# Kernel optimization log

Hardware: AMD Instinct MI355X
Metric: run time of the kernel (lower is better)

The kernel has to match this reference:

```python
import jax, jax.numpy as jnp
import numpy as np

GRID_SIZE = 5
SPLINE_ORDER = 3
GRID_MIN = -1.0
GRID_MAX = 1.0
H = (GRID_MAX - GRID_MIN) / GRID_SIZE          # grid interval
G0 = GRID_MIN - SPLINE_ORDER * H               # first (extended) knot = grid[:,0]


def _basis_matrix():
    # Uniform B-spline power-basis matrix, same recurrence as the torch code.
    M = np.array([[1.0]], dtype=np.float64)
    scalar = 1.0
    for k in range(2, SPLINE_ORDER + 2):
        t1 = np.pad(M, ((0, 1), (0, 0)))
        t3 = np.pad(M, ((1, 0), (0, 0)))
        t2 = np.zeros((k - 1, k))
        t4 = np.zeros((k - 1, k))
        for i in range(k - 1):
            t2[i, i] = i + 1
            t2[i, i + 1] = k - (i + 2)
            t4[i, i] = -1.0
            t4[i, i + 1] = 1.0
        M = t1 @ t2 + t3 @ t4
        scalar *= 1.0 / (k - 1)
    return (M * scalar).astype(np.float32)

BASIS = jnp.asarray(_basis_matrix())  # (spline_order+1, spline_order+1)


def setup_inputs():
    key = jax.random.key(0)
    k1, k2, k3 = jax.random.split(key, 3)
    N, FIN, FOUT = 2048, 128, 128
    x = jax.random.normal(k1, (N, FIN), dtype=jnp.float32)
    base_weight = jax.random.normal(k2, (FOUT, FIN), dtype=jnp.float32) * 0.1
    spline_weight = jax.random.normal(k3, (FIN, FOUT, GRID_SIZE + SPLINE_ORDER), dtype=jnp.float32) * 0.1
    return {"x": x, "base_weight": base_weight, "spline_weight": spline_weight}


def _forward(x, base_weight, spline_weight):
    N, fin = x.shape
    fout = base_weight.shape[0]
    k = SPLINE_ORDER
    # base branch: SiLU activation then linear
    base_out = jax.nn.silu(x) @ base_weight.T                       # (N, fout)
    # input normalization: Hardtanh around grid center (shift=0, scale=1 for [-1,1])
    shift = (GRID_MIN + GRID_MAX) / 2.0
    scale = (GRID_MAX - GRID_MIN) / 2.0
    xn = jnp.clip((x - shift) / scale, -1.0, 1.0) * scale + shift
    # bucketize: bin index + fractional position (replaces floor/compare + torch.nonzero)
    t = (xn - G0) / H
    fl = jnp.floor(t)
    u1 = t - fl                                                     # (x - interval_floor) / interval
    idx = jnp.clip(fl.astype(jnp.int32), k, k + GRID_SIZE - 1)      # clamped knot-interval index
    cfloor = idx - k                                                # (N, fin) first control point index
    # power bases [1, u, u^2, ..., u^k] -> b-spline basis via basis matrix
    pows = u1[..., None] ** jnp.arange(k + 1, dtype=x.dtype)        # (N, fin, k+1)
    bspl = pows @ BASIS.astype(x.dtype)                             # (N, fin, k+1)
    # faithful to torch: spline_weight.view(out, in, -1) memory reinterpretation
    cp = jnp.reshape(spline_weight, (fout, fin, GRID_SIZE + k))
    gidx = cfloor[..., None] + jnp.arange(k + 1)                    # (N, fin, k+1) control point indices
    i_idx = jnp.arange(fin)[None, :, None]
    gathered = cp[:, i_idx, gidx]                                   # (fout, N, fin, k+1)
    gathered = jnp.transpose(gathered, (1, 0, 2, 3))                # (N, fout, fin, k+1)
    # faithful to torch: .view(N, in, k+1, out) memory reinterpretation
    cpr = jnp.reshape(gathered, (N, fin, k + 1, fout))
    # per-feature spline matmul then sum over in_features (KAN aggregation)
    spline_out = jnp.einsum('nij,nijo->no', bspl, cpr)              # (N, fout)
    return base_out + spline_out


def reference(x, base_weight, spline_weight):
    return _forward(x, base_weight, spline_weight)
```

## Files before the change

kernel.cpp:

```cpp
#include <hip/hip_runtime.h>
#include <hip/hip_bf16.h>
#include <math.h>

typedef __attribute__((ext_vector_type(8))) short short8;
typedef __attribute__((ext_vector_type(4))) float floatx4;

static __device__ __forceinline__ unsigned short bfbits(float f) {
    __hip_bfloat16 h = __float2bfloat16(f);
    unsigned short u;
    __builtin_memcpy(&u, &h, 2);
    return u;
}
static __device__ __forceinline__ unsigned pack2(float lo, float hi) {
    return (unsigned)bfbits(lo) | ((unsigned)bfbits(hi) << 16);
}

#define SP_STR  136
#define SBN_STR 76
#define SBB_STR 136
#define ST_STR  68
#define SC_STR  132

__global__ __launch_bounds__(256) void kan_fused(
    const float* __restrict__ x,
    const float* __restrict__ bw,
    const float* __restrict__ sw,
    float* __restrict__ out)
{
    __shared__ short sP[5 * 16 * SP_STR];
    __shared__ short sBn[2][128 * SBN_STR];
    __shared__ short sBb[32 * SBB_STR];
    __shared__ float sT[2][16 * ST_STR];
    __shared__ unsigned char sC[16 * SC_STR];

    const int tid = threadIdx.x;
    const int nb  = blockIdx.x >> 2;
    const int s   = blockIdx.x & 3;
    const int n0  = nb * 16;

    const int ar = tid >> 4;
    const int sg = tid & 15;

    const int r  = tid >> 4;
    const int i0 = (tid & 15) * 8;
    float v[8];
    *(float4*)(v)     = *(const float4*)(x + (n0 + r) * 128 + i0);
    *(float4*)(v + 4) = *(const float4*)(x + (n0 + r) * 128 + i0 + 4);

    float4 pre[8];
#pragma unroll
    for (int rr = 0; rr < 8; ++rr)
        pre[rr] = *(const float4*)(sw + (ar + 16 * rr) * 1024 + s * 64 + sg * 4);

    {
        float A5[5][8];
        unsigned char cc8[8];
#pragma unroll
        for (int i = 0; i < 8; ++i) {
            float xv = v[i];
            float si = xv / (1.0f + expf(-xv));
            float xn = fminf(fmaxf(xv, -1.0f), 1.0f);
            float t  = (xn + 2.2f) / 0.4f;
            float u  = t - floorf(t);
            int idx  = (int)floorf(t);
            idx = min(max(idx, 3), 7);
            cc8[i] = (unsigned char)(idx - 3);
            float u2 = u * u, u3 = u2 * u, om = 1.0f - u;
            A5[0][i] = om * om * om * (1.0f / 6.0f);
            A5[1][i] = 0.5f * u3 - u2 + (2.0f / 3.0f);
            A5[2][i] = -0.5f * u3 + 0.5f * u2 + 0.5f * u + (1.0f / 6.0f);
            A5[3][i] = u3 * (1.0f / 6.0f);
            A5[4][i] = si;
        }
#pragma unroll
        for (int g = 0; g < 5; ++g) {
            unsigned p0 = pack2(A5[g][0], A5[g][1]);
            unsigned p1 = pack2(A5[g][2], A5[g][3]);
            unsigned p2 = pack2(A5[g][4], A5[g][5]);
            unsigned p3 = pack2(A5[g][6], A5[g][7]);
            *(uint4*)(&sP[(g * 16 + r) * SP_STR + i0]) = make_uint4(p0, p1, p2, p3);
        }
        *(unsigned*)(&sC[r * SC_STR + i0])     = cc8[0] | (cc8[1]<<8) | (cc8[2]<<16) | (cc8[3]<<24);
        *(unsigned*)(&sC[r * SC_STR + i0 + 4]) = cc8[4] | (cc8[5]<<8) | (cc8[6]<<16) | (cc8[7]<<24);
    }

    const int w = tid >> 6, l = tid & 63;
    const int m = l & 15, q = l >> 4;
    const int gn  = tid >> 4;
    const int go2 = tid & 15;

    uint2 pk[8];
#pragma unroll
    for (int rr = 0; rr < 8; ++rr)
        pk[rr] = make_uint2(pack2(pre[rr].x, pre[rr].y), pack2(pre[rr].z, pre[rr].w));

    float racc0 = 0.f, racc1 = 0.f;
    float4 bpre[4];

#pragma unroll
    for (int t = 0; t < 4; ++t) {
        const int p = t & 1;
#pragma unroll
        for (int rr = 0; rr < 8; ++rr)
            *(uint2*)(&sBn[p][(ar + 16 * rr) * SBN_STR + sg * 4]) = pk[rr];
        __syncthreads();

        if (t < 3) {
#pragma unroll
            for (int rr = 0; rr < 8; ++rr)
                pre[rr] = *(const float4*)(sw + (ar + 16 * rr) * 1024 + (s + 4 * (t + 1)) * 64 + sg * 4);
        } else {
#pragma unroll
            for (int i = 0; i < 4; ++i) {
                int e = i * 256 + tid;
                bpre[i] = *(const float4*)(bw + (32 * s + (e >> 5)) * 128 + (e & 31) * 4);
            }
        }

        if (t > 0) {
            int oh  = 8 * s + (go2 >> 1);
            int c   = sC[gn * SC_STR + 32 * (t - 1) + oh];
            int rel = 8 * (go2 >> 1) + c + 2 * (go2 & 1);
            racc0 += sT[1 - p][gn * ST_STR + rel];
            racc1 += sT[1 - p][gn * ST_STR + rel + 1];
        }

        floatx4 acc = {0.f, 0.f, 0.f, 0.f};
#pragma unroll
        for (int kk = 0; kk < 4; ++kk) {
            short8 af = *(const short8*)(&sP[(t * 16 + m) * SP_STR + q * 8 + kk * 32]);
            short8 bf;
#pragma unroll
            for (int j2 = 0; j2 < 8; ++j2)
                bf[j2] = sBn[p][(kk * 32 + q * 8 + j2) * SBN_STR + 16 * w + m];
            acc = __builtin_amdgcn_mfma_f32_16x16x32_bf16(af, bf, acc, 0, 0, 0);
        }
#pragma unroll
        for (int rr = 0; rr < 4; ++rr)
            sT[p][(q * 4 + rr) * ST_STR + 16 * w + m] = acc[rr];

        if (t < 3) {
#pragma unroll
            for (int rr = 0; rr < 8; ++rr)
                pk[rr] = make_uint2(pack2(pre[rr].x, pre[rr].y), pack2(pre[rr].z, pre[rr].w));
        }
    }

#pragma unroll
    for (int i = 0; i < 4; ++i) {
        int e = i * 256 + tid;
        *(uint2*)(&sBb[(e >> 5) * SBB_STR + (e & 31) * 4]) =
            make_uint2(pack2(bpre[i].x, bpre[i].y), pack2(bpre[i].z, bpre[i].w));
    }
    __syncthreads();

    {
        int oh  = 8 * s + (go2 >> 1);
        int c   = sC[gn * SC_STR + 32 * 3 + oh];
        int rel = 8 * (go2 >> 1) + c + 2 * (go2 & 1);
        racc0 += sT[1][gn * ST_STR + rel];
        racc1 += sT[1][gn * ST_STR + rel + 1];
    }

    if (w < 2) {
        floatx4 acc = {0.f, 0.f, 0.f, 0.f};
#pragma unroll
        for (int kk = 0; kk < 4; ++kk) {
            short8 af = *(const short8*)(&sP[(4 * 16 + m) * SP_STR + q * 8 + kk * 32]);
            short8 bf = *(const short8*)(&sBb[(16 * w + m) * SBB_STR + q * 8 + kk * 32]);
            acc = __builtin_amdgcn_mfma_f32_16x16x32_bf16(af, bf, acc, 0, 0, 0);
        }
#pragma unroll
        for (int rr = 0; rr < 4; ++rr)
            sT[0][(q * 4 + rr) * ST_STR + 16 * w + m] = acc[rr];
    }
    __syncthreads();

    racc0 += sT[0][gn * ST_STR + 2 * go2];
    racc1 += sT[0][gn * ST_STR + 2 * go2 + 1];

    *(float2*)(out + (n0 + gn) * 128 + 32 * s + 2 * go2) = make_float2(racc0, racc1);
}

extern "C" void kernel_launch(void* const* d_in, const int* in_sizes, int n_in,
                              void* d_out, int out_size, void* d_ws, size_t ws_size,
                              hipStream_t stream) {
    const float* x  = (const float*)d_in[0];
    const float* bw = (const float*)d_in[1];
    const float* sw = (const float*)d_in[2];
    float* out = (float*)d_out;
    kan_fused<<<dim3(512), dim3(256), 0, stream>>>(x, bw, sw, out);
}
```

Before: 63.49 us.

## Single-buffer spline weight tile in LDS and cut prefetch registers for occupancy

Drops the double-buffered sBn tile and the separate base-weight buffer, reusing one LDS buffer for every spline slice and for the base weights. Only half of each next weight slice is prefetched into registers; the other half is loaded synchronously after the MFMA step. Launch bounds now request three blocks per SM. The aim is lower LDS and register use so more blocks stay resident, at the cost of an extra barrier per iteration and less overlap of global loads with compute.

```diff
diff --git a/kernel.cpp b/kernel.cpp
--- a/kernel.cpp
+++ b/kernel.cpp
@@ -21,15 +21,14 @@
 #define ST_STR  68
 #define SC_STR  132
 
-__global__ __launch_bounds__(256) void kan_fused(
+__global__ __launch_bounds__(256, 3) void kan_fused(
     const float* __restrict__ x,
     const float* __restrict__ bw,
     const float* __restrict__ sw,
     float* __restrict__ out)
 {
     __shared__ short sP[5 * 16 * SP_STR];
-    __shared__ short sBn[2][128 * SBN_STR];
-    __shared__ short sBb[32 * SBB_STR];
+    __shared__ short sBn[128 * SBN_STR];
     __shared__ float sT[2][16 * ST_STR];
     __shared__ unsigned char sC[16 * SC_STR];
 
@@ -47,9 +46,9 @@
     *(float4*)(v)     = *(const float4*)(x + (n0 + r) * 128 + i0);
     *(float4*)(v + 4) = *(const float4*)(x + (n0 + r) * 128 + i0 + 4);
 
-    float4 pre[8];
-#pragma unroll
-    for (int rr = 0; rr < 8; ++rr)
+    float4 pre[4];
+#pragma unroll
+    for (int rr = 0; rr < 4; ++rr)
         pre[rr] = *(const float4*)(sw + (ar + 16 * rr) * 1024 + s * 64 + sg * 4);
 
     {
@@ -84,15 +83,24 @@
         *(unsigned*)(&sC[r * SC_STR + i0 + 4]) = cc8[4] | (cc8[5]<<8) | (cc8[6]<<16) | (cc8[7]<<24);
     }
 
+#pragma unroll
+    for (int rr = 0; rr < 4; ++rr)
+        *(uint2*)(&sBn[(ar + 16 * rr) * SBN_STR + sg * 4]) =
+            make_uint2(pack2(pre[rr].x, pre[rr].y), pack2(pre[rr].z, pre[rr].w));
+#pragma unroll
+    for (int rr = 4; rr < 8; ++rr) {
+        float4 h = *(const float4*)(sw + (ar + 16 * rr) * 1024 + s * 64 + sg * 4);
+        *(uint2*)(&sBn[(ar + 16 * rr) * SBN_STR + sg * 4]) =
+            make_uint2(pack2(h.x, h.y), pack2(h.z, h.w));
+    }
+    __syncthreads();
+
     const int w = tid >> 6, l = tid & 63;
     const int m = l & 15, q = l >> 4;
     const int gn  = tid >> 4;
     const int go2 = tid & 15;
-
-    uint2 pk[8];
-#pragma unroll
-    for (int rr = 0; rr < 8; ++rr)
-        pk[rr] = make_uint2(pack2(pre[rr].x, pre[rr].y), pack2(pre[rr].z, pre[rr].w));
+    const int oh  = 8 * s + (go2 >> 1);
+    const int oloc = 8 * (go2 >> 1) + 2 * (go2 & 1);
 
     float racc0 = 0.f, racc1 = 0.f;
     float4 bpre[4];
@@ -100,14 +108,10 @@
 #pragma unroll
     for (int t = 0; t < 4; ++t) {
         const int p = t & 1;
-#pragma unroll
-        for (int rr = 0; rr < 8; ++rr)
-            *(uint2*)(&sBn[p][(ar + 16 * rr) * SBN_STR + sg * 4]) = pk[rr];
-        __syncthreads();
 
         if (t < 3) {
 #pragma unroll
-            for (int rr = 0; rr < 8; ++rr)
+            for (int rr = 0; rr < 4; ++rr)
                 pre[rr] = *(const float4*)(sw + (ar + 16 * rr) * 1024 + (s + 4 * (t + 1)) * 64 + sg * 4);
         } else {
 #pragma unroll
@@ -118,9 +122,8 @@
         }
 
         if (t > 0) {
-            int oh  = 8 * s + (go2 >> 1);
             int c   = sC[gn * SC_STR + 32 * (t - 1) + oh];
-            int rel = 8 * (go2 >> 1) + c + 2 * (go2 & 1);
+            int rel = oloc + c;
             racc0 += sT[1 - p][gn * ST_STR + rel];
             racc1 += sT[1 - p][gn * ST_STR + rel + 1];
         }
@@ -132,50 +135,57 @@
             short8 bf;
 #pragma unroll
             for (int j2 = 0; j2 < 8; ++j2)
-                bf[j2] = sBn[p][(kk * 32 + q * 8 + j2) * SBN_STR + 16 * w + m];
+                bf[j2] = sBn[(kk * 32 + q * 8 + j2) * SBN_STR + 16 * w + m];
             acc = __builtin_amdgcn_mfma_f32_16x16x32_bf16(af, bf, acc, 0, 0, 0);
         }
 #pragma unroll
         for (int rr = 0; rr < 4; ++rr)
             sT[p][(q * 4 + rr) * ST_STR + 16 * w + m] = acc[rr];
 
+        __syncthreads();
+
         if (t < 3) {
 #pragma unroll
-            for (int rr = 0; rr < 8; ++rr)
-                pk[rr] = make_uint2(pack2(pre[rr].x, pre[rr].y), pack2(pre[rr].z, pre[rr].w));
-        }
-    }
-
-#pragma unroll
-    for (int i = 0; i < 4; ++i) {
-        int e = i * 256 + tid;
-        *(uint2*)(&sBb[(e >> 5) * SBB_STR + (e & 31) * 4]) =
-            make_uint2(pack2(bpre[i].x, bpre[i].y), pack2(bpre[i].z, bpre[i].w));
+            for (int rr = 0; rr < 4; ++rr)
+                *(uint2*)(&sBn[(ar + 16 * rr) * SBN_STR + sg * 4]) =
+                    make_uint2(pack2(pre[rr].x, pre[rr].y), pack2(pre[rr].z, pre[rr].w));
+#pragma unroll
+            for (int rr = 4; rr < 8; ++rr) {
+                float4 h = *(const float4*)(sw + (ar + 16 * rr) * 1024 + (s + 4 * (t + 1)) * 64 + sg * 4);
+                *(uint2*)(&sBn[(ar + 16 * rr) * SBN_STR + sg * 4]) =
+                    make_uint2(pack2(h.x, h.y), pack2(h.z, h.w));
+            }
+        } else {
+#pragma unroll
+            for (int i = 0; i < 4; ++i) {
+                int e = i * 256 + tid;
+                *(uint2*)(&sBn[(e >> 5) * SBB_STR + (e & 31) * 4]) =
+                    make_uint2(pack2(bpre[i].x, bpre[i].y), pack2(bpre[i].z, bpre[i].w));
+            }
+        }
+        __syncthreads();
+    }
+
+    if (w < 2) {
+        floatx4 acc = {0.f, 0.f, 0.f, 0.f};
+#pragma unroll
+        for (int kk = 0; kk < 4; ++kk) {
+            short8 af = *(const short8*)(&sP[(4 * 16 + m) * SP_STR + q * 8 + kk * 32]);
+            short8 bf = *(const short8*)(&sBn[(16 * w + m) * SBB_STR + q * 8 + kk * 32]);
+            acc = __builtin_amdgcn_mfma_f32_16x16x32_bf16(af, bf, acc, 0, 0, 0);
+        }
+#pragma unroll
+        for (int rr = 0; rr < 4; ++rr)
+            sT[0][(q * 4 + rr) * ST_STR + 16 * w + m] = acc[rr];
     }
     __syncthreads();
 
     {
-        int oh  = 8 * s + (go2 >> 1);
         int c   = sC[gn * SC_STR + 32 * 3 + oh];
-        int rel = 8 * (go2 >> 1) + c + 2 * (go2 & 1);
+        int rel = oloc + c;
         racc0 += sT[1][gn * ST_STR + rel];
         racc1 += sT[1][gn * ST_STR + rel + 1];
     }
-
-    if (w < 2) {
-        floatx4 acc = {0.f, 0.f, 0.f, 0.f};
-#pragma unroll
-        for (int kk = 0; kk < 4; ++kk) {
-            short8 af = *(const short8*)(&sP[(4 * 16 + m) * SP_STR + q * 8 + kk * 32]);
-            short8 bf = *(const short8*)(&sBb[(16 * w + m) * SBB_STR + q * 8 + kk * 32]);
-            acc = __builtin_amdgcn_mfma_f32_16x16x32_bf16(af, bf, acc, 0, 0, 0);
-        }
-#pragma unroll
-        for (int rr = 0; rr < 4; ++rr)
-            sT[0][(q * 4 + rr) * ST_STR + 16 * w + m] = acc[rr];
-    }
-    __syncthreads();
-
     racc0 += sT[0][gn * ST_STR + 2 * go2];
     racc1 += sT[0][gn * ST_STR + 2 * go2 + 1];
 
```

Result: no change. 64.68 us (median of 2 runs) (+1.9%).
